# Optimization experiments

Measured on AMD Instinct MI355X. Metric: run time of the kernel, lower is better.

Reference implementation:

```python
import jax, jax.numpy as jnp
import numpy as np

NEG_SLOPE = 0.2


def gat_conv(x, src, dst, W, att_src, att_dst, bias, heads, out_ch, concat):
    """PyG-style GATConv (eval mode, self-loops already appended to src/dst)."""
    N = x.shape[0]
    h = (x @ W).reshape(N, heads, out_ch)                      # [N,H,C]
    a_src = jnp.einsum('nhc,hc->nh', h, att_src)               # [N,H]
    a_dst = jnp.einsum('nhc,hc->nh', h, att_dst)               # [N,H]
    e = jax.nn.leaky_relu(a_src[src] + a_dst[dst], NEG_SLOPE)  # [E,H]
    # numerically-stable softmax segmented by destination node
    emax = jax.ops.segment_max(e, dst, num_segments=N)         # [N,H]
    e = jnp.exp(e - emax[dst])
    denom = jax.ops.segment_sum(e, dst, num_segments=N)
    alpha = e / (denom[dst] + 1e-16)                           # [E,H]
    msg = h[src] * alpha[..., None]                            # [E,H,C]
    out = jax.ops.segment_sum(msg, dst, num_segments=N)        # [N,H,C]
    out = out.reshape(N, heads * out_ch) if concat else out.mean(axis=1)
    return out + bias


def setup_inputs() -> dict:
    key = jax.random.key(0)
    ks = jax.random.split(key, 9)
    N, E, IN, OUT = 100000, 1600000, 128, 40
    H1, C1 = 8, 8
    x = jax.random.normal(ks[0], (N, IN), dtype=jnp.float32)
    edge_index = jax.random.randint(ks[1], (2, E), 0, N, dtype=jnp.int64)
    s = 0.1
    return {
        'x': x,
        'edge_index': edge_index,
        'W1': jax.random.normal(ks[2], (IN, H1 * C1), dtype=jnp.float32) * s,
        'att_src1': jax.random.normal(ks[3], (H1, C1), dtype=jnp.float32) * s,
        'att_dst1': jax.random.normal(ks[4], (H1, C1), dtype=jnp.float32) * s,
        'b1': jnp.zeros((H1 * C1,), dtype=jnp.float32),
        'W2': jax.random.normal(ks[5], (H1 * C1, OUT), dtype=jnp.float32) * s,
        'att_src2': jax.random.normal(ks[6], (1, OUT), dtype=jnp.float32) * s,
        'att_dst2': jax.random.normal(ks[7], (1, OUT), dtype=jnp.float32) * s,
        'b2': jnp.zeros((OUT,), dtype=jnp.float32),
    }


def reference(x, edge_index, W1, att_src1, att_dst1, b1, W2, att_src2, att_dst2, b2):
    N = x.shape[0]
    loops = jnp.arange(N, dtype=edge_index.dtype)
    src = jnp.concatenate([edge_index[0], loops])  # self-loops (PyG default)
    dst = jnp.concatenate([edge_index[1], loops])
    h = gat_conv(x, src, dst, W1, att_src1, att_dst1, b1, 8, 8, True)
    h = jax.nn.elu(h)  # dropout is identity in eval mode
    out = gat_conv(h, src, dst, W2, att_src2, att_dst2, b2, 1, W2.shape[1], False)
    return jax.nn.log_softmax(out, axis=-1)
```

## Files before the change

kernel.cpp:

```cpp
#include <hip/hip_runtime.h>
#include <math.h>

#define NEG_SLOPE 0.2f
#define BSHIFT 8
#define MAXBUK 512

typedef __attribute__((ext_vector_type(8))) short short8;
typedef __attribute__((ext_vector_type(4))) float floatx4;

static __device__ __forceinline__ float lrelu_exp(float e) {
    e = fmaxf(e, NEG_SLOPE * e);
    return __expf(e);
}

static __device__ __forceinline__ short f2bf(float f) {
    union { float f; unsigned u; } v; v.f = f;
    unsigned r = v.u + 0x7FFFu + ((v.u >> 16) & 1u);
    return (short)(r >> 16);
}
static __device__ __forceinline__ float bf2f(unsigned short s) {
    union { float f; unsigned u; } v;
    v.u = ((unsigned)s) << 16;
    return v.f;
}
static __device__ __forceinline__ float bfpair_lo(unsigned v) {
    union { float f; unsigned u; } x; x.u = v << 16; return x.f;
}
static __device__ __forceinline__ float bfpair_hi(unsigned v) {
    union { float f; unsigned u; } x; x.u = v & 0xffff0000u; return x.f;
}
static __device__ __forceinline__ void splitbf(float f, short& hi, short& lo) {
    hi = f2bf(f);
    lo = f2bf(f - bf2f((unsigned short)hi));
}


__global__ __launch_bounds__(512) void k_hist(const int* __restrict__ dst, int E, int CHUNK,
                                              int NBLK, int NBUK, int* __restrict__ blockhist) {
    __shared__ int hist[MAXBUK];
    int t = threadIdx.x, b = blockIdx.x;
    for (int i = t; i < NBUK; i += 512) hist[i] = 0;
    __syncthreads();
    int e0 = b * CHUNK, e1 = e0 + CHUNK; if (e1 > E) e1 = E;
    for (int e = e0 + t; e < e1; e += 512) atomicAdd(&hist[dst[e] >> BSHIFT], 1);
    __syncthreads();
    for (int i = t; i < NBUK; i += 512) blockhist[(size_t)i * NBLK + b] = hist[i];
}

__global__ __launch_bounds__(256) void k_colscan(int* __restrict__ blockhist,
                                                 int* __restrict__ btot, int NBLK) {
    int bucket = blockIdx.x, t = threadIdx.x;
    int lane = t & 63, wv = t >> 6;
    __shared__ int wsum[4];
    __shared__ int carry_s;
    if (t == 0) carry_s = 0;
    __syncthreads();
    for (int base = 0; base < NBLK; base += 256) {
        int idx = base + t;
        int v = (idx < NBLK) ? blockhist[(size_t)bucket * NBLK + idx] : 0;
        int s = v;
#pragma unroll
        for (int o = 1; o < 64; o <<= 1) {
            int u = __shfl_up(s, o, 64);
            if (lane >= o) s += u;
        }
        if (lane == 63) wsum[wv] = s;
        __syncthreads();
        int b0 = 0;
#pragma unroll
        for (int w = 0; w < 4; ++w) b0 += (w < wv) ? wsum[w] : 0;
        int excl = s + b0 - v + carry_s;
        if (idx < NBLK) blockhist[(size_t)bucket * NBLK + idx] = excl;
        __syncthreads();
        if (t == 255) carry_s += s + b0;
        __syncthreads();
    }
    if (t == 0) btot[bucket] = carry_s;
}

__global__ __launch_bounds__(512) void k_bucket_scan(const int* __restrict__ btot,
                                                     int* __restrict__ bucketbase, int NBUK) {
    __shared__ int sh[512];
    int t = threadIdx.x;
    int v = (t < NBUK) ? btot[t] : 0;
    sh[t] = v;
    __syncthreads();
#pragma unroll
    for (int o = 1; o < 512; o <<= 1) {
        int u = (t >= o) ? sh[t - o] : 0;
        __syncthreads();
        sh[t] += u;
        __syncthreads();
    }
    if (t < NBUK) bucketbase[t] = sh[t] - v;
    if (t == NBUK - 1) bucketbase[NBUK] = sh[t];
}

__global__ __launch_bounds__(512) void k_partition(const int* __restrict__ src,
                                                   const int* __restrict__ dst, int E, int CHUNK,
                                                   int NBLK, int NBUK,
                                                   const int* __restrict__ blockhist,
                                                   const int* __restrict__ bucketbase,
                                                   unsigned* __restrict__ packed) {
    __shared__ int cur[MAXBUK];
    int t = threadIdx.x, b = blockIdx.x;
    for (int i = t; i < NBUK; i += 512)
        cur[i] = blockhist[(size_t)i * NBLK + b] + bucketbase[i];
    __syncthreads();
    int e0 = b * CHUNK, e1 = e0 + CHUNK; if (e1 > E) e1 = E;
    for (int e = e0 + t; e < e1; e += 512) {
        int d = dst[e], s = src[e];
        int pos = atomicAdd(&cur[d >> BSHIFT], 1);
        packed[pos] = ((unsigned)s << 8) | ((unsigned)d & 255u);
    }
}

__global__ __launch_bounds__(256) void k_fine(const unsigned* __restrict__ packed,
                                              const int* __restrict__ bucketbase,
                                              int* __restrict__ offsets,
                                              int* __restrict__ csr_src,
                                              int N, int NBUK) {
    __shared__ int fcnt[256];
    __shared__ int wsum[4];
    int bucket = blockIdx.x, t = threadIdx.x;
    int lo = bucket << BSHIFT;
    int nn = N - lo; if (nn > 256) nn = 256;
    int ebase = bucketbase[bucket];
    int ecnt = bucketbase[bucket + 1] - ebase;
    fcnt[t] = 0;
    __syncthreads();
    for (int i = t; i < ecnt; i += 256) {
        unsigned p = packed[ebase + i];
        atomicAdd(&fcnt[p & 255u], 1);
    }
    __syncthreads();
    int v = fcnt[t];
    int lane = t & 63, wv = t >> 6;
    int s = v;
#pragma unroll
    for (int o = 1; o < 64; o <<= 1) {
        int u = __shfl_up(s, o, 64);
        if (lane >= o) s += u;
    }
    if (lane == 63) wsum[wv] = s;
    __syncthreads();
    int base = 0;
#pragma unroll
    for (int w = 0; w < 4; ++w) base += (w < wv) ? wsum[w] : 0;
    int excl = s + base - v;
    if (t < nn) offsets[lo + t] = ebase + excl;
    if (bucket == NBUK - 1 && t == 0) offsets[N] = ebase + ecnt;
    __syncthreads();
    fcnt[t] = excl;
    __syncthreads();
    for (int i = t; i < ecnt; i += 256) {
        unsigned p = packed[ebase + i];
        int pos = atomicAdd(&fcnt[p & 255u], 1);
        csr_src[ebase + pos] = (int)(p >> 8);
    }
}

__global__ __launch_bounds__(256) void k_splitW2(const float* __restrict__ W2,
                                                 short* __restrict__ w2h,
                                                 short* __restrict__ w2l) {
    int i = blockIdx.x * 256 + threadIdx.x;
    if (i < 64 * 48) {
        int row = i / 48, col = i % 48;
        short hi = 0, lo = 0;
        if (col < 40) splitbf(W2[row * 40 + col], hi, lo);
        w2h[i] = hi; w2l[i] = lo;
    }
}

__global__ __launch_bounds__(256) void k_gemm1(const float* __restrict__ x,
                                               const float* __restrict__ W1,
                                               const float* __restrict__ att_s,
                                               const float* __restrict__ att_d,
                                               unsigned short* __restrict__ h1b,
                                               float* __restrict__ a_s1,
                                               float* __restrict__ a_d1, int N) {
    int tid = threadIdx.x, wave = tid >> 6, lane = tid & 63;
    int n16 = lane & 15, q = lane >> 4;
    int nb = blockIdx.x * 64 + wave * 16;
    if (nb >= N) return;

    short8 bfr[4][4];
#pragma unroll
    for (int ct = 0; ct < 4; ++ct) {
        int n = ct * 16 + n16;
#pragma unroll
        for (int kc = 0; kc < 4; ++kc) {
            int k0 = kc * 32 + q * 8;
            short8 b;
#pragma unroll
            for (int j = 0; j < 8; ++j) b[j] = f2bf(W1[(k0 + j) * 64 + n]);
            bfr[ct][kc] = b;
        }
    }

    int arow = nb + n16; if (arow >= N) arow = N - 1;
    const float* xr = x + (size_t)arow * 128 + q * 8;
    short8 afr[4];
#pragma unroll
    for (int kc = 0; kc < 4; ++kc) {
        float4 u0 = *(const float4*)(xr + kc * 32);
        float4 u1 = *(const float4*)(xr + kc * 32 + 4);
        short8 a;
        a[0] = f2bf(u0.x); a[1] = f2bf(u0.y); a[2] = f2bf(u0.z); a[3] = f2bf(u0.w);
        a[4] = f2bf(u1.x); a[5] = f2bf(u1.y); a[6] = f2bf(u1.z); a[7] = f2bf(u1.w);
        afr[kc] = a;
    }

    floatx4 acc[4];
#pragma unroll
    for (int ct = 0; ct < 4; ++ct) {
        floatx4 c = {0.f, 0.f, 0.f, 0.f};
#pragma unroll
        for (int kc = 0; kc < 4; ++kc)
            c = __builtin_amdgcn_mfma_f32_16x16x32_bf16(afr[kc], bfr[ct][kc], c, 0, 0, 0);
        acc[ct] = c;
    }

#pragma unroll
    for (int ct = 0; ct < 4; ++ct) {
#pragma unroll
        for (int r = 0; r < 4; ++r) {
            int row = nb + q * 4 + r;
            if (row < N) h1b[(size_t)row * 64 + ct * 16 + n16] = (unsigned short)f2bf(acc[ct][r]);
        }
    }

#pragma unroll
    for (int ct = 0; ct < 4; ++ct) {
        float as = att_s[ct * 16 + n16];
        float ad = att_d[ct * 16 + n16];
#pragma unroll
        for (int r = 0; r < 4; ++r) {
            float ps = acc[ct][r] * as;
            float pd = acc[ct][r] * ad;
#pragma unroll
            for (int m = 1; m < 8; m <<= 1) {
                ps += __shfl_xor(ps, m, 64);
                pd += __shfl_xor(pd, m, 64);
            }
            int row = nb + q * 4 + r;
            if ((n16 & 7) == 0 && row < N) {
                int h = 2 * ct + (n16 >> 3);
                a_s1[row * 8 + h] = ps;
                a_d1[row * 8 + h] = pd;
            }
        }
    }
}

__global__ __launch_bounds__(256) void k_agg1(const unsigned short* __restrict__ h1b,
                                              const float* __restrict__ a_s1,
                                              const float* __restrict__ a_d1,
                                              const int* __restrict__ offsets,
                                              const int* __restrict__ csr_src,
                                              const float* __restrict__ b1,
                                              float* __restrict__ y1, int N) {
    int wave = threadIdx.x >> 6, lane = threadIdx.x & 63;
    int d = blockIdx.x * 4 + wave;
    if (d >= N) return;
    int g = lane >> 3;
    int h = lane & 7;
    float ad = a_d1[d * 8 + h];
    float acc[8] = {0.f, 0.f, 0.f, 0.f, 0.f, 0.f, 0.f, 0.f};
    float wsum_l = 0.f;
    if (g == 0) {
        float w0 = lrelu_exp(a_s1[d * 8 + h] + ad);
        uint4 v = *(const uint4*)(h1b + (size_t)d * 64 + 8 * h);
        acc[0] = w0 * bfpair_lo(v.x); acc[1] = w0 * bfpair_hi(v.x);
        acc[2] = w0 * bfpair_lo(v.y); acc[3] = w0 * bfpair_hi(v.y);
        acc[4] = w0 * bfpair_lo(v.z); acc[5] = w0 * bfpair_hi(v.z);
        acc[6] = w0 * bfpair_lo(v.w); acc[7] = w0 * bfpair_hi(v.w);
        wsum_l = w0;
    }
    int i0 = offsets[d], i1 = offsets[d + 1];
    for (int base = i0; base < i1; base += 64) {
        int m = i1 - base; if (m > 64) m = 64;
        int sv = (lane < m) ? csr_src[base + lane] : 0;
        for (int j = 0; j < m; j += 16) {
            int eA = j + g;
            int siA = __shfl(sv, eA, 64);
            bool liveB = (j + 8 < m);
            if (liveB) {
                int eB = j + 8 + g;
                int siB = __shfl(sv, eB, 64);
                float evA = a_s1[siA * 8 + h] + ad;
                float evB = a_s1[siB * 8 + h] + ad;
                uint4 vA = *(const uint4*)(h1b + (size_t)siA * 64 + 8 * h);
                uint4 vB = *(const uint4*)(h1b + (size_t)siB * 64 + 8 * h);
                float wA = (eA < m) ? lrelu_exp(evA) : 0.f;
                float wB = (eB < m) ? lrelu_exp(evB) : 0.f;
                wsum_l += wA + wB;
                acc[0] = fmaf(wA, bfpair_lo(vA.x), acc[0]);
                acc[1] = fmaf(wA, bfpair_hi(vA.x), acc[1]);
                acc[2] = fmaf(wA, bfpair_lo(vA.y), acc[2]);
                acc[3] = fmaf(wA, bfpair_hi(vA.y), acc[3]);
                acc[4] = fmaf(wA, bfpair_lo(vA.z), acc[4]);
                acc[5] = fmaf(wA, bfpair_hi(vA.z), acc[5]);
                acc[6] = fmaf(wA, bfpair_lo(vA.w), acc[6]);
                acc[7] = fmaf(wA, bfpair_hi(vA.w), acc[7]);
                acc[0] = fmaf(wB, bfpair_lo(vB.x), acc[0]);
                acc[1] = fmaf(wB, bfpair_hi(vB.x), acc[1]);
                acc[2] = fmaf(wB, bfpair_lo(vB.y), acc[2]);
                acc[3] = fmaf(wB, bfpair_hi(vB.y), acc[3]);
                acc[4] = fmaf(wB, bfpair_lo(vB.z), acc[4]);
                acc[5] = fmaf(wB, bfpair_hi(vB.z), acc[5]);
                acc[6] = fmaf(wB, bfpair_lo(vB.w), acc[6]);
                acc[7] = fmaf(wB, bfpair_hi(vB.w), acc[7]);
            } else {
                float evA = a_s1[siA * 8 + h] + ad;
                uint4 vA = *(const uint4*)(h1b + (size_t)siA * 64 + 8 * h);
                float wA = (eA < m) ? lrelu_exp(evA) : 0.f;
                wsum_l += wA;
                acc[0] = fmaf(wA, bfpair_lo(vA.x), acc[0]);
                acc[1] = fmaf(wA, bfpair_hi(vA.x), acc[1]);
                acc[2] = fmaf(wA, bfpair_lo(vA.y), acc[2]);
                acc[3] = fmaf(wA, bfpair_hi(vA.y), acc[3]);
                acc[4] = fmaf(wA, bfpair_lo(vA.z), acc[4]);
                acc[5] = fmaf(wA, bfpair_hi(vA.z), acc[5]);
                acc[6] = fmaf(wA, bfpair_lo(vA.w), acc[6]);
                acc[7] = fmaf(wA, bfpair_hi(vA.w), acc[7]);
            }
        }
    }
#pragma unroll
    for (int mm = 8; mm < 64; mm <<= 1) {
#pragma unroll
        for (int k = 0; k < 8; ++k) acc[k] += __shfl_xor(acc[k], mm, 64);
        wsum_l += __shfl_xor(wsum_l, mm, 64);
    }
    if (g == 0) {
        float inv = 1.f / (wsum_l + 1e-16f);
        float4 bA = *(const float4*)(b1 + 8 * h);
        float4 bB = *(const float4*)(b1 + 8 * h + 4);
        float o[8];
        o[0] = acc[0] * inv + bA.x;
        o[1] = acc[1] * inv + bA.y;
        o[2] = acc[2] * inv + bA.z;
        o[3] = acc[3] * inv + bA.w;
        o[4] = acc[4] * inv + bB.x;
        o[5] = acc[5] * inv + bB.y;
        o[6] = acc[6] * inv + bB.z;
        o[7] = acc[7] * inv + bB.w;
#pragma unroll
        for (int k = 0; k < 8; ++k) o[k] = o[k] > 0.f ? o[k] : (__expf(o[k]) - 1.f);
        float4 s0 = make_float4(o[0], o[1], o[2], o[3]);
        float4 s1 = make_float4(o[4], o[5], o[6], o[7]);
        *(float4*)(y1 + (size_t)d * 64 + 8 * h) = s0;
        *(float4*)(y1 + (size_t)d * 64 + 8 * h + 4) = s1;
    }
}

__global__ __launch_bounds__(256) void k_gemm2(const float* __restrict__ y1,
                                               const short* __restrict__ w2h,
                                               const short* __restrict__ w2l,
                                               const float* __restrict__ att_s,
                                               const float* __restrict__ att_d,
                                               unsigned short* __restrict__ h2b,
                                               float* __restrict__ a2s,
                                               float* __restrict__ a2d, int N) {
    int tid = threadIdx.x, wave = tid >> 6, lane = tid & 63;
    int n16 = lane & 15, q = lane >> 4;
    int nb = blockIdx.x * 64 + wave * 16;
    if (nb >= N) return;

    int arow = nb + n16; if (arow >= N) arow = N - 1;
    const float* yr = y1 + (size_t)arow * 64 + q * 8;
    short8 ah[2], al[2];
#pragma unroll
    for (int kc = 0; kc < 2; ++kc) {
        float4 u0 = *(const float4*)(yr + kc * 32);
        float4 u1 = *(const float4*)(yr + kc * 32 + 4);
        short8 h, l; short hi, lo;
        splitbf(u0.x, hi, lo); h[0] = hi; l[0] = lo;
        splitbf(u0.y, hi, lo); h[1] = hi; l[1] = lo;
        splitbf(u0.z, hi, lo); h[2] = hi; l[2] = lo;
        splitbf(u0.w, hi, lo); h[3] = hi; l[3] = lo;
        splitbf(u1.x, hi, lo); h[4] = hi; l[4] = lo;
        splitbf(u1.y, hi, lo); h[5] = hi; l[5] = lo;
        splitbf(u1.z, hi, lo); h[6] = hi; l[6] = lo;
        splitbf(u1.w, hi, lo); h[7] = hi; l[7] = lo;
        ah[kc] = h; al[kc] = l;
    }

    float psr[4] = {0.f, 0.f, 0.f, 0.f}, pdr[4] = {0.f, 0.f, 0.f, 0.f};
#pragma unroll
    for (int ct = 0; ct < 3; ++ct) {
        int n = ct * 16 + n16;
        short8 bh0, bh1, bl0, bl1;
#pragma unroll
        for (int j = 0; j < 8; ++j) {
            int k0 = q * 8 + j;
            bh0[j] = w2h[k0 * 48 + n];
            bl0[j] = w2l[k0 * 48 + n];
            bh1[j] = w2h[(32 + k0) * 48 + n];
            bl1[j] = w2l[(32 + k0) * 48 + n];
        }
        floatx4 c = {0.f, 0.f, 0.f, 0.f};
        c = __builtin_amdgcn_mfma_f32_16x16x32_bf16(ah[0], bl0, c, 0, 0, 0);
        c = __builtin_amdgcn_mfma_f32_16x16x32_bf16(al[0], bh0, c, 0, 0, 0);
        c = __builtin_amdgcn_mfma_f32_16x16x32_bf16(ah[0], bh0, c, 0, 0, 0);
        c = __builtin_amdgcn_mfma_f32_16x16x32_bf16(ah[1], bl1, c, 0, 0, 0);
        c = __builtin_amdgcn_mfma_f32_16x16x32_bf16(al[1], bh1, c, 0, 0, 0);
        c = __builtin_amdgcn_mfma_f32_16x16x32_bf16(ah[1], bh1, c, 0, 0, 0);

        int col = ct * 16 + n16;
#pragma unroll
        for (int r = 0; r < 4; ++r) {
            int row = nb + q * 4 + r;
            if (col < 40 && row < N) h2b[(size_t)row * 40 + col] = (unsigned short)f2bf(c[r]);
        }
        float asv = (col < 40) ? att_s[col] : 0.f;
        float adv = (col < 40) ? att_d[col] : 0.f;
#pragma unroll
        for (int r = 0; r < 4; ++r) {
            psr[r] = fmaf(c[r], asv, psr[r]);
            pdr[r] = fmaf(c[r], adv, pdr[r]);
        }
    }
#pragma unroll
    for (int r = 0; r < 4; ++r) {
        float ps = psr[r], pd = pdr[r];
#pragma unroll
        for (int m = 1; m < 16; m <<= 1) {
            ps += __shfl_xor(ps, m, 64);
            pd += __shfl_xor(pd, m, 64);
        }
        int row = nb + q * 4 + r;
        if (n16 == 0 && row < N) { a2s[row] = ps; a2d[row] = pd; }
    }
}

__global__ __launch_bounds__(256) void k_agg2(const unsigned short* __restrict__ h2b,
                                              const float* __restrict__ a2s,
                                              const float* __restrict__ a2d,
                                              const int* __restrict__ offsets,
                                              const int* __restrict__ csr_src,
                                              const float* __restrict__ b2,
                                              float* __restrict__ out, int N) {
    int wave = threadIdx.x >> 6, lane = threadIdx.x & 63;
    int q = lane >> 4;
    int ll = lane & 15;
    int d = (blockIdx.x * 4 + wave) * 4 + q;
    bool dvalid = (d < N);
    int de = dvalid ? d : N - 1;
    int g = ll / 5;
    int c = ll - g * 5;
    bool lane_ok = (ll < 15);
    float ad = a2d[de];
    float w0 = lrelu_exp(a2s[de] + ad);
    int i0 = offsets[de];
    int deg = offsets[de + 1] - i0;
    if (!dvalid) deg = 0;
    int dmax = deg;
    dmax = max(dmax, __shfl_xor(dmax, 16, 64));
    dmax = max(dmax, __shfl_xor(dmax, 32, 64));
    float acc[8] = {0.f, 0.f, 0.f, 0.f, 0.f, 0.f, 0.f, 0.f};
    float wsum_l = 0.f;
    if (g == 0) {
        uint4 v = *(const uint4*)(h2b + (size_t)de * 40 + 8 * c);
        acc[0] = w0 * bfpair_lo(v.x); acc[1] = w0 * bfpair_hi(v.x);
        acc[2] = w0 * bfpair_lo(v.y); acc[3] = w0 * bfpair_hi(v.y);
        acc[4] = w0 * bfpair_lo(v.z); acc[5] = w0 * bfpair_hi(v.z);
        acc[6] = w0 * bfpair_lo(v.w); acc[7] = w0 * bfpair_hi(v.w);
    }
    for (int j = 0; j < dmax; j += 6) {
        int jA = j + g, jB = j + 3 + g;
        bool liveA = lane_ok && (jA < deg);
        bool liveB = lane_ok && (jB < deg);
        int svA = de, svB = de;
        if (liveA) svA = csr_src[i0 + jA];
        if (liveB) svB = csr_src[i0 + jB];
        float eA = a2s[svA] + ad;
        float eB = a2s[svB] + ad;
        uint4 vA = *(const uint4*)(h2b + (size_t)svA * 40 + 8 * c);
        uint4 vB = *(const uint4*)(h2b + (size_t)svB * 40 + 8 * c);
        float wA = liveA ? lrelu_exp(eA) : 0.f;
        float wB = liveB ? lrelu_exp(eB) : 0.f;
        if (c == 0) wsum_l += wA + wB;
        acc[0] = fmaf(wA, bfpair_lo(vA.x), acc[0]);
        acc[1] = fmaf(wA, bfpair_hi(vA.x), acc[1]);
        acc[2] = fmaf(wA, bfpair_lo(vA.y), acc[2]);
        acc[3] = fmaf(wA, bfpair_hi(vA.y), acc[3]);
        acc[4] = fmaf(wA, bfpair_lo(vA.z), acc[4]);
        acc[5] = fmaf(wA, bfpair_hi(vA.z), acc[5]);
        acc[6] = fmaf(wA, bfpair_lo(vA.w), acc[6]);
        acc[7] = fmaf(wA, bfpair_hi(vA.w), acc[7]);
        acc[0] = fmaf(wB, bfpair_lo(vB.x), acc[0]);
        acc[1] = fmaf(wB, bfpair_hi(vB.x), acc[1]);
        acc[2] = fmaf(wB, bfpair_lo(vB.y), acc[2]);
        acc[3] = fmaf(wB, bfpair_hi(vB.y), acc[3]);
        acc[4] = fmaf(wB, bfpair_lo(vB.z), acc[4]);
        acc[5] = fmaf(wB, bfpair_hi(vB.z), acc[5]);
        acc[6] = fmaf(wB, bfpair_lo(vB.w), acc[6]);
        acc[7] = fmaf(wB, bfpair_hi(vB.w), acc[7]);
    }
#pragma unroll
    for (int k = 0; k < 8; ++k)
        acc[k] += __shfl(acc[k], lane + 5, 64) + __shfl(acc[k], lane + 10, 64);
    wsum_l += __shfl(wsum_l, lane + 5, 64) + __shfl(wsum_l, lane + 10, 64);
    wsum_l = __shfl(wsum_l, lane & 48, 64);
    float wsum = wsum_l + w0;
    bool act5 = (ll < 5) && dvalid;
    float inv = 1.f / (wsum + 1e-16f);
    float4 bA = *(const float4*)(b2 + 8 * c);
    float4 bB = *(const float4*)(b2 + 8 * c + 4);
    float o[8];
    o[0] = acc[0] * inv + bA.x;
    o[1] = acc[1] * inv + bA.y;
    o[2] = acc[2] * inv + bA.z;
    o[3] = acc[3] * inv + bA.w;
    o[4] = acc[4] * inv + bB.x;
    o[5] = acc[5] * inv + bB.y;
    o[6] = acc[6] * inv + bB.z;
    o[7] = acc[7] * inv + bB.w;
    float mxl = -INFINITY;
    if (act5) {
        mxl = fmaxf(fmaxf(fmaxf(o[0], o[1]), fmaxf(o[2], o[3])),
                    fmaxf(fmaxf(o[4], o[5]), fmaxf(o[6], o[7])));
    }
#pragma unroll
    for (int mm = 1; mm < 8; mm <<= 1) mxl = fmaxf(mxl, __shfl_xor(mxl, mm, 64));
    float exl = 0.f;
    if (act5) {
#pragma unroll
        for (int k = 0; k < 8; ++k) exl += __expf(o[k] - mxl);
    }
#pragma unroll
    for (int mm = 1; mm < 8; mm <<= 1) exl += __shfl_xor(exl, mm, 64);
    if (act5) {
        float lse = mxl + __logf(exl);
        float4 s0 = make_float4(o[0] - lse, o[1] - lse, o[2] - lse, o[3] - lse);
        float4 s1 = make_float4(o[4] - lse, o[5] - lse, o[6] - lse, o[7] - lse);
        *(float4*)(out + (size_t)d * 40 + 8 * c) = s0;
        *(float4*)(out + (size_t)d * 40 + 8 * c + 4) = s1;
    }
}


extern "C" void kernel_launch(void* const* d_in, const int* in_sizes, int n_in,
                              void* d_out, int out_size, void* d_ws, size_t ws_size,
                              hipStream_t stream) {
    const float* x   = (const float*)d_in[0];
    const int*   ei  = (const int*)d_in[1];
    const float* W1  = (const float*)d_in[2];
    const float* as1 = (const float*)d_in[3];
    const float* ad1 = (const float*)d_in[4];
    const float* b1  = (const float*)d_in[5];
    const float* W2  = (const float*)d_in[6];
    const float* as2 = (const float*)d_in[7];
    const float* ad2 = (const float*)d_in[8];
    const float* b2  = (const float*)d_in[9];
    float* out = (float*)d_out;

    int N = in_sizes[0] / 128;
    int E = in_sizes[1] / 2;
    const int* src = ei;
    const int* dst = ei + E;

    int NBUK = (N + 255) >> BSHIFT;
    int CHUNK = 4096;
    int NBLK = (E + CHUNK - 1) / CHUNK;

    char* ws = (char*)d_ws;
    size_t off = 0;
    auto alloc = [&](size_t bytes) -> char* {
        char* p = ws + off;
        off += (bytes + 255) & ~(size_t)255;
        return p;
    };
    unsigned short* h1b = (unsigned short*)alloc((size_t)N * 64 * 2);
    float* a_s1    = (float*)alloc((size_t)N * 8 * 4);
    float* a_d1    = (float*)alloc((size_t)N * 8 * 4);
    float* y1      = (float*)alloc((size_t)N * 64 * 4);
    size_t shared_sz = (size_t)N * 40 * 2;
    if ((size_t)E * 4 > shared_sz) shared_sz = (size_t)E * 4;
    char*  region  = alloc(shared_sz);
    unsigned short* h2b = (unsigned short*)region;
    unsigned* packed    = (unsigned*)region;
    float* a2s     = (float*)alloc((size_t)N * 4);
    float* a2d     = (float*)alloc((size_t)N * 4);
    int*   offsets = (int*)alloc((size_t)(N + 1) * 4);
    int*   csr_src = (int*)alloc((size_t)E * 4);
    int*   blockhist  = (int*)alloc((size_t)NBUK * NBLK * 4);
    int*   btot       = (int*)alloc((size_t)NBUK * 4);
    int*   bucketbase = (int*)alloc((size_t)(NBUK + 1) * 4);
    short* w2h     = (short*)alloc((size_t)64 * 48 * 2);
    short* w2l     = (short*)alloc((size_t)64 * 48 * 2);

    int nb = (N + 3) / 4;
    int nb2 = (N + 15) / 16;
    int gb = (N + 63) / 64;

    k_hist<<<NBLK, 512, 0, stream>>>(dst, E, CHUNK, NBLK, NBUK, blockhist);
    k_colscan<<<NBUK, 256, 0, stream>>>(blockhist, btot, NBLK);
    k_bucket_scan<<<1, 512, 0, stream>>>(btot, bucketbase, NBUK);
    k_partition<<<NBLK, 512, 0, stream>>>(src, dst, E, CHUNK, NBLK, NBUK, blockhist,
                                          bucketbase, packed);
    k_fine<<<NBUK, 256, 0, stream>>>(packed, bucketbase, offsets, csr_src, N, NBUK);
    k_splitW2<<<12, 256, 0, stream>>>(W2, w2h, w2l);
    k_gemm1<<<gb, 256, 0, stream>>>(x, W1, as1, ad1, h1b, a_s1, a_d1, N);
    k_agg1<<<nb, 256, 0, stream>>>(h1b, a_s1, a_d1, offsets, csr_src, b1, y1, N);
    k_gemm2<<<gb, 256, 0, stream>>>(y1, w2h, w2l, as2, ad2, h2b, a2s, a2d, N);
    k_agg2<<<nb2, 256, 0, stream>>>(h2b, a2s, a2d, offsets, csr_src, b2, out, N);
}
```

Baseline: 172.6 us.

## Process four destination nodes per wave in layer-1 aggregation

The layer-1 aggregation kernel now assigns a 16-lane quarter-wave to each destination node instead of a full wave per node. Each quarter loops over that node's edges two at a time per half, loading source indices directly rather than staging them through shuffles, and finishes with a single shuffle reduction. This targets idle lanes, since average degree is about 16 and whole-wave chunks of 64 leave most lanes unused. In exchange, per-wave divergence grows with the largest of the four degrees, and each lane issues more serial gather iterations.

```diff
diff --git a/kernel.cpp b/kernel.cpp
--- a/kernel.cpp
+++ b/kernel.cpp
@@ -261,82 +261,68 @@
                                               const float* __restrict__ b1,
                                               float* __restrict__ y1, int N) {
     int wave = threadIdx.x >> 6, lane = threadIdx.x & 63;
-    int d = blockIdx.x * 4 + wave;
-    if (d >= N) return;
-    int g = lane >> 3;
-    int h = lane & 7;
-    float ad = a_d1[d * 8 + h];
+    int q = lane >> 4;
+    int ll = lane & 15;
+    int d = (blockIdx.x * 4 + wave) * 4 + q;
+    bool dvalid = (d < N);
+    int de = dvalid ? d : N - 1;
+    int g = ll >> 3;
+    int c = ll & 7;
+    float ad = a_d1[de * 8 + c];
+    int i0 = offsets[de];
+    int deg = dvalid ? (offsets[de + 1] - i0) : 0;
+    int dmax = deg;
+    dmax = max(dmax, __shfl_xor(dmax, 16, 64));
+    dmax = max(dmax, __shfl_xor(dmax, 32, 64));
     float acc[8] = {0.f, 0.f, 0.f, 0.f, 0.f, 0.f, 0.f, 0.f};
     float wsum_l = 0.f;
     if (g == 0) {
-        float w0 = lrelu_exp(a_s1[d * 8 + h] + ad);
-        uint4 v = *(const uint4*)(h1b + (size_t)d * 64 + 8 * h);
+        float w0 = lrelu_exp(a_s1[de * 8 + c] + ad);
+        uint4 v = *(const uint4*)(h1b + (size_t)de * 64 + 8 * c);
         acc[0] = w0 * bfpair_lo(v.x); acc[1] = w0 * bfpair_hi(v.x);
         acc[2] = w0 * bfpair_lo(v.y); acc[3] = w0 * bfpair_hi(v.y);
         acc[4] = w0 * bfpair_lo(v.z); acc[5] = w0 * bfpair_hi(v.z);
         acc[6] = w0 * bfpair_lo(v.w); acc[7] = w0 * bfpair_hi(v.w);
         wsum_l = w0;
     }
-    int i0 = offsets[d], i1 = offsets[d + 1];
-    for (int base = i0; base < i1; base += 64) {
-        int m = i1 - base; if (m > 64) m = 64;
-        int sv = (lane < m) ? csr_src[base + lane] : 0;
-        for (int j = 0; j < m; j += 16) {
-            int eA = j + g;
-            int siA = __shfl(sv, eA, 64);
-            bool liveB = (j + 8 < m);
-            if (liveB) {
-                int eB = j + 8 + g;
-                int siB = __shfl(sv, eB, 64);
-                float evA = a_s1[siA * 8 + h] + ad;
-                float evB = a_s1[siB * 8 + h] + ad;
-                uint4 vA = *(const uint4*)(h1b + (size_t)siA * 64 + 8 * h);
-                uint4 vB = *(const uint4*)(h1b + (size_t)siB * 64 + 8 * h);
-                float wA = (eA < m) ? lrelu_exp(evA) : 0.f;
-                float wB = (eB < m) ? lrelu_exp(evB) : 0.f;
-                wsum_l += wA + wB;
-                acc[0] = fmaf(wA, bfpair_lo(vA.x), acc[0]);
-                acc[1] = fmaf(wA, bfpair_hi(vA.x), acc[1]);
-                acc[2] = fmaf(wA, bfpair_lo(vA.y), acc[2]);
-                acc[3] = fmaf(wA, bfpair_hi(vA.y), acc[3]);
-                acc[4] = fmaf(wA, bfpair_lo(vA.z), acc[4]);
-                acc[5] = fmaf(wA, bfpair_hi(vA.z), acc[5]);
-                acc[6] = fmaf(wA, bfpair_lo(vA.w), acc[6]);
-                acc[7] = fmaf(wA, bfpair_hi(vA.w), acc[7]);
-                acc[0] = fmaf(wB, bfpair_lo(vB.x), acc[0]);
-                acc[1] = fmaf(wB, bfpair_hi(vB.x), acc[1]);
-                acc[2] = fmaf(wB, bfpair_lo(vB.y), acc[2]);
-                acc[3] = fmaf(wB, bfpair_hi(vB.y), acc[3]);
-                acc[4] = fmaf(wB, bfpair_lo(vB.z), acc[4]);
-                acc[5] = fmaf(wB, bfpair_hi(vB.z), acc[5]);
-                acc[6] = fmaf(wB, bfpair_lo(vB.w), acc[6]);
-                acc[7] = fmaf(wB, bfpair_hi(vB.w), acc[7]);
-            } else {
-                float evA = a_s1[siA * 8 + h] + ad;
-                uint4 vA = *(const uint4*)(h1b + (size_t)siA * 64 + 8 * h);
-                float wA = (eA < m) ? lrelu_exp(evA) : 0.f;
-                wsum_l += wA;
-                acc[0] = fmaf(wA, bfpair_lo(vA.x), acc[0]);
-                acc[1] = fmaf(wA, bfpair_hi(vA.x), acc[1]);
-                acc[2] = fmaf(wA, bfpair_lo(vA.y), acc[2]);
-                acc[3] = fmaf(wA, bfpair_hi(vA.y), acc[3]);
-                acc[4] = fmaf(wA, bfpair_lo(vA.z), acc[4]);
-                acc[5] = fmaf(wA, bfpair_hi(vA.z), acc[5]);
-                acc[6] = fmaf(wA, bfpair_lo(vA.w), acc[6]);
-                acc[7] = fmaf(wA, bfpair_hi(vA.w), acc[7]);
-            }
-        }
-    }
-#pragma unroll
-    for (int mm = 8; mm < 64; mm <<= 1) {
-#pragma unroll
-        for (int k = 0; k < 8; ++k) acc[k] += __shfl_xor(acc[k], mm, 64);
-        wsum_l += __shfl_xor(wsum_l, mm, 64);
-    }
-    if (g == 0) {
+    for (int j = 0; j < dmax; j += 4) {
+        int jA = j + g, jB = j + 2 + g;
+        bool liveA = (jA < deg);
+        bool liveB = (jB < deg);
+        int svA = de, svB = de;
+        if (liveA) svA = csr_src[i0 + jA];
+        if (liveB) svB = csr_src[i0 + jB];
+        float eA = a_s1[svA * 8 + c] + ad;
+        float eB = a_s1[svB * 8 + c] + ad;
+        uint4 vA = *(const uint4*)(h1b + (size_t)svA * 64 + 8 * c);
+        uint4 vB = *(const uint4*)(h1b + (size_t)svB * 64 + 8 * c);
+        float wA = liveA ? lrelu_exp(eA) : 0.f;
+        float wB = liveB ? lrelu_exp(eB) : 0.f;
+        wsum_l += wA + wB;
+        acc[0] = fmaf(wA, bfpair_lo(vA.x), acc[0]);
+        acc[1] = fmaf(wA, bfpair_hi(vA.x), acc[1]);
+        acc[2] = fmaf(wA, bfpair_lo(vA.y), acc[2]);
+        acc[3] = fmaf(wA, bfpair_hi(vA.y), acc[3]);
+        acc[4] = fmaf(wA, bfpair_lo(vA.z), acc[4]);
+        acc[5] = fmaf(wA, bfpair_hi(vA.z), acc[5]);
+        acc[6] = fmaf(wA, bfpair_lo(vA.w), acc[6]);
+        acc[7] = fmaf(wA, bfpair_hi(vA.w), acc[7]);
+        acc[0] = fmaf(wB, bfpair_lo(vB.x), acc[0]);
+        acc[1] = fmaf(wB, bfpair_hi(vB.x), acc[1]);
+        acc[2] = fmaf(wB, bfpair_lo(vB.y), acc[2]);
+        acc[3] = fmaf(wB, bfpair_hi(vB.y), acc[3]);
+        acc[4] = fmaf(wB, bfpair_lo(vB.z), acc[4]);
+        acc[5] = fmaf(wB, bfpair_hi(vB.z), acc[5]);
+        acc[6] = fmaf(wB, bfpair_lo(vB.w), acc[6]);
+        acc[7] = fmaf(wB, bfpair_hi(vB.w), acc[7]);
+    }
+#pragma unroll
+    for (int k = 0; k < 8; ++k) acc[k] += __shfl(acc[k], lane + 8, 64);
+    wsum_l += __shfl(wsum_l, lane + 8, 64);
+    if (g == 0 && dvalid) {
         float inv = 1.f / (wsum_l + 1e-16f);
-        float4 bA = *(const float4*)(b1 + 8 * h);
-        float4 bB = *(const float4*)(b1 + 8 * h + 4);
+        float4 bA = *(const float4*)(b1 + 8 * c);
+        float4 bB = *(const float4*)(b1 + 8 * c + 4);
         float o[8];
         o[0] = acc[0] * inv + bA.x;
         o[1] = acc[1] * inv + bA.y;
@@ -350,8 +336,8 @@
         for (int k = 0; k < 8; ++k) o[k] = o[k] > 0.f ? o[k] : (__expf(o[k]) - 1.f);
         float4 s0 = make_float4(o[0], o[1], o[2], o[3]);
         float4 s1 = make_float4(o[4], o[5], o[6], o[7]);
-        *(float4*)(y1 + (size_t)d * 64 + 8 * h) = s0;
-        *(float4*)(y1 + (size_t)d * 64 + 8 * h + 4) = s1;
+        *(float4*)(y1 + (size_t)d * 64 + 8 * c) = s0;
+        *(float4*)(y1 + (size_t)d * 64 + 8 * c + 4) = s1;
     }
 }
 
@@ -592,7 +578,7 @@
     short* w2h     = (short*)alloc((size_t)64 * 48 * 2);
     short* w2l     = (short*)alloc((size_t)64 * 48 * 2);
 
-    int nb = (N + 3) / 4;
+    int nb1 = (N + 15) / 16;
     int nb2 = (N + 15) / 16;
     int gb = (N + 63) / 64;
 
@@ -604,7 +590,7 @@
     k_fine<<<NBUK, 256, 0, stream>>>(packed, bucketbase, offsets, csr_src, N, NBUK);
     k_splitW2<<<12, 256, 0, stream>>>(W2, w2h, w2l);
     k_gemm1<<<gb, 256, 0, stream>>>(x, W1, as1, ad1, h1b, a_s1, a_d1, N);
-    k_agg1<<<nb, 256, 0, stream>>>(h1b, a_s1, a_d1, offsets, csr_src, b1, y1, N);
+    k_agg1<<<nb1, 256, 0, stream>>>(h1b, a_s1, a_d1, offsets, csr_src, b1, y1, N);
     k_gemm2<<<gb, 256, 0, stream>>>(y1, w2h, w2l, as2, ad2, h2b, a2s, a2d, N);
     k_agg2<<<nb2, 256, 0, stream>>>(h2b, a2s, a2d, offsets, csr_src, b2, out, N);
 }
```

After: 171.2 us. Within noise of the previous version (-0.9%).
